# Performance work log

Hardware: AMD Instinct MI355X
Metric: run time of the kernel (lower is better)

The kernel has to match this reference:

```python
import jax, jax.numpy as jnp
import numpy as np

B, T, N = 256, 512, 256
START, STOP = 254, 255


def setup_inputs() -> dict:
    key = jax.random.key(0)
    k1, k2, k3 = jax.random.split(key, 3)
    inputs = jax.random.normal(k1, (B, T, N), dtype=jnp.float32)
    transitions = jax.random.normal(k2, (N, N), dtype=jnp.float32)
    # sentinel rows/cols as in __init__
    transitions = transitions.at[START, :].set(-10000.0).at[:, STOP].set(-10000.0)
    tags = jax.random.randint(k3, (B, T), 0, N, dtype=jnp.int32)
    mask = jnp.ones((B, T), dtype=jnp.int32)
    return {"inputs": inputs, "transitions": transitions, "tags": tags, "mask": mask}


def _input_likelihood(inputs, transitions, fmask):
    # alpha[b, tag]: log-sum over paths ending at tag
    alpha0 = transitions[:, START][None, :] + inputs[:, 0, :]

    def step(alpha, xs):
        emit, m = xs  # emit: (B, N), m: (B,)
        # inner[b, next, prev] = alpha[b, prev] + (emit[b, next] + trans[next, prev]) * mask[b, i-1]
        inner = alpha[:, None, :] + (emit[:, :, None] + transitions[None, :, :]) * m[:, None, None]
        return jax.nn.logsumexp(inner, axis=-1), None

    xs = (jnp.swapaxes(inputs[:, 1:, :], 0, 1), jnp.swapaxes(fmask[:, :-1], 0, 1))
    alpha, _ = jax.lax.scan(step, alpha0, xs)
    stops = alpha + transitions[STOP][None, :]
    return jax.nn.logsumexp(stops, axis=-1)  # (B,)


def _joint_likelihood(inputs, transitions, tags, fmask):
    score = transitions[tags[:, 0], START]  # (B,)
    # transitions[next, prev] * mask[:, i+1], summed over steps
    trans_sc = transitions[tags[:, 1:], tags[:, :-1]] * fmask[:, 1:]
    # inputs[b, i, prev_tag] * mask[:, i]
    emit_sc = jnp.take_along_axis(inputs[:, :-1, :], tags[:, :-1, None], axis=2)[..., 0] * fmask[:, :-1]
    score = score + trans_sc.sum(axis=-1) + emit_sc.sum(axis=-1)
    last_idx = (fmask.sum(axis=-1) - 1.0).astype(jnp.int32)  # (B,)
    last_tags = jnp.take_along_axis(tags, last_idx[:, None], axis=1)[:, 0]
    last_input = jnp.take_along_axis(inputs[:, -1, :], last_tags[:, None], axis=1)[:, 0]
    return score + transitions[STOP, last_tags] + last_input * fmask[:, -1]


def reference(inputs, transitions, tags, mask):
    fmask = mask.astype(jnp.float32)
    log_denominator = _input_likelihood(inputs, transitions, fmask)
    log_numerator = _joint_likelihood(inputs, transitions, tags, fmask)
    return jnp.sum(log_numerator - log_denominator)
```

## Files before the change

### kernel.cpp

```cpp
#include <hip/hip_runtime.h>
#include <hip/hip_bf16.h>
#include <stdint.h>

#define B_    256
#define T_    512
#define N_    256
#define START_ 254
#define STOP_  255
#define GCOLS 16
#define NF    16
#define ND    32
#define LOG2E 1.4426950408889634f
#define LN2   0.6931471805599453f
#define VP8   272

#define WSB_OFF 65536
#define WCF_OFF 131072
#define WCB_OFF 131328

typedef __attribute__((ext_vector_type(4))) float floatx4;

__device__ __forceinline__ void lds_barrier() {
    asm volatile("s_waitcnt lgkmcnt(0)\n\ts_barrier" ::: "memory");
}

__device__ __forceinline__ int pk_fp8x4(float a, float b, float c, float d) {
    int r = __builtin_amdgcn_cvt_pk_fp8_f32(a, b, 0, false);
    return __builtin_amdgcn_cvt_pk_fp8_f32(c, d, r, true);
}
__device__ __forceinline__ int pk_bf8x4(float a, float b, float c, float d) {
    int r = __builtin_amdgcn_cvt_pk_bf8_f32(a, b, 0, false);
    return __builtin_amdgcn_cvt_pk_bf8_f32(c, d, r, true);
}
__device__ __forceinline__ long long mk64(int lo, int hi) {
    return ((long long)(unsigned long long)(unsigned)hi << 32) | (unsigned)lo;
}

struct DenomShared {
    alignas(16) char V[2][GCOLS * VP8];
    alignas(16) float mbuf[GCOLS * 8];
    alignas(16) float sbuf[GCOLS * 8];
};

template<bool ISF>
__device__ __forceinline__ void denom_path(
    DenomShared& sh, const float* __restrict__ inputs,
    const float* __restrict__ trans, const int* __restrict__ mask,
    float* __restrict__ ws, int blkLocal)
{
    const int tid = threadIdx.x;
    const int w = tid >> 6;
    const int l = tid & 63;
    const int q = l >> 4;
    const int b = l & 15;
    const int bg = blkLocal * GCOLS + b;
    const int j0 = 32 * w + 4 * q;
    const int S = ISF ? 256 : 255;

    auto EIDX = [](int s) { return ISF ? s : (511 - s); };
    auto MIDX = [](int s) { return ISF ? (s - 1) : (511 - s); };

    long long afrag[2][8];
    #pragma unroll
    for (int mt = 0; mt < 2; ++mt) {
        const int row = 32 * w + 16 * mt + b;
        #pragma unroll
        for (int kt = 0; kt < 8; ++kt) {
            float e[8];
            if (ISF) {
                const float* p = trans + row * N_ + kt * 32 + q * 8;
                floatx4 t0 = *(const floatx4*)p;
                floatx4 t1 = *(const floatx4*)(p + 4);
                #pragma unroll
                for (int jj = 0; jj < 4; ++jj) {
                    e[jj]     = __builtin_amdgcn_exp2f(t0[jj] * LOG2E);
                    e[jj + 4] = __builtin_amdgcn_exp2f(t1[jj] * LOG2E);
                }
            } else {
                #pragma unroll
                for (int jj = 0; jj < 8; ++jj) {
                    const int k = kt * 32 + q * 8 + jj;
                    e[jj] = __builtin_amdgcn_exp2f(trans[k * N_ + row] * LOG2E);
                }
            }
            afrag[mt][kt] = mk64(pk_fp8x4(e[0], e[1], e[2], e[3]),
                                 pk_fp8x4(e[4], e[5], e[6], e[7]));
        }
    }

    const float* emitp = inputs + (size_t)bg * T_ * N_;
    const int*   maskp = mask + bg * T_;
    float C = 0.f;
    float u[2][4];

    auto produce = [&]() {
        float mx = u[0][0], sm = 0.f;
        #pragma unroll
        for (int mt = 0; mt < 2; ++mt)
            #pragma unroll
            for (int r = 0; r < 4; ++r) { mx = fmaxf(mx, u[mt][r]); sm += u[mt][r]; }
        mx = fmaxf(mx, __shfl_xor(mx, 16, 64)); sm += __shfl_xor(sm, 16, 64);
        mx = fmaxf(mx, __shfl_xor(mx, 32, 64)); sm += __shfl_xor(sm, 32, 64);
        if (l < 16) { sh.mbuf[b * 8 + w] = mx; sh.sbuf[b * 8 + w] = sm; }
    };

    if (ISF) {
        #pragma unroll
        for (int mt = 0; mt < 2; ++mt) {
            floatx4 em = *(const floatx4*)(emitp + j0 + 16 * mt);
            #pragma unroll
            for (int r = 0; r < 4; ++r) {
                const int j = j0 + 16 * mt + r;
                u[mt][r] = __builtin_amdgcn_exp2f((trans[j * N_ + START_] + em[r]) * LOG2E);
            }
        }
    } else {
        #pragma unroll
        for (int mt = 0; mt < 2; ++mt) {
            floatx4 st = *(const floatx4*)(trans + STOP_ * N_ + j0 + 16 * mt);
            #pragma unroll
            for (int r = 0; r < 4; ++r)
                u[mt][r] = __builtin_amdgcn_exp2f(st[r] * LOG2E);
        }
    }
    {
        float xpi[2][4] = {{1.f,1.f,1.f,1.f},{1.f,1.f,1.f,1.f}};
        if (!ISF) {
            #pragma unroll
            for (int mt = 0; mt < 2; ++mt) {
                floatx4 e = *(const floatx4*)(emitp + (size_t)511 * N_ + j0 + 16 * mt);
                #pragma unroll
                for (int r = 0; r < 4; ++r)
                    xpi[mt][r] = __builtin_amdgcn_exp2f(e[r] * LOG2E);
            }
        }
        produce();
        #pragma unroll
        for (int mt = 0; mt < 2; ++mt)
            *(int*)&sh.V[0][b * VP8 + j0 + 16 * mt] =
                pk_bf8x4(u[mt][0] * xpi[mt][0], u[mt][1] * xpi[mt][1],
                         u[mt][2] * xpi[mt][2], u[mt][3] * xpi[mt][3]);
    }
    floatx4 eA[2], eB[2];
    eA[0] = *(const floatx4*)(emitp + (size_t)EIDX(1) * N_ + j0);
    eA[1] = *(const floatx4*)(emitp + (size_t)EIDX(1) * N_ + j0 + 16);
    eB[0] = *(const floatx4*)(emitp + (size_t)EIDX(2) * N_ + j0);
    eB[1] = *(const floatx4*)(emitp + (size_t)EIDX(2) * N_ + j0 + 16);
    float mA = (float)maskp[MIDX(1)];
    float mB = (float)maskp[MIDX(2)];
    lds_barrier();

    auto body = [&](int s, int pr) {
        const int sp = (s + 2 <= S) ? s + 2 : S;
        floatx4 eC0 = *(const floatx4*)(emitp + (size_t)EIDX(sp) * N_ + j0);
        floatx4 eC1 = *(const floatx4*)(emitp + (size_t)EIDX(sp) * N_ + j0 + 16);
        const float mC = (float)maskp[MIDX(sp)];

        const char* vb = &sh.V[pr][b * VP8];
        long long bf[8];
        #pragma unroll
        for (int kt = 0; kt < 8; ++kt)
            bf[kt] = *(const long long*)(vb + kt * 32 + q * 8);

        floatx4 m0 = *(const floatx4*)&sh.mbuf[b * 8];
        floatx4 m1 = *(const floatx4*)&sh.mbuf[b * 8 + 4];
        floatx4 s0 = *(const floatx4*)&sh.sbuf[b * 8];
        floatx4 s1 = *(const floatx4*)&sh.sbuf[b * 8 + 4];
        const float cmax = fmaxf(fmaxf(fmaxf(m0[0], m0[1]), fmaxf(m0[2], m0[3])),
                                 fmaxf(fmaxf(m1[0], m1[1]), fmaxf(m1[2], m1[3])));
        const float csum = ((s0[0] + s0[1]) + (s0[2] + s0[3])) +
                           ((s1[0] + s1[1]) + (s1[2] + s1[3]));
        const uint32_t cb = __builtin_bit_cast(uint32_t, cmax);
        const int eb = (int)((cb >> 23) & 0xFFu);
        const float rs = __builtin_bit_cast(float, (uint32_t)(249 - eb) << 23);

        float xpv[2][4];
        #pragma unroll
        for (int r = 0; r < 4; ++r) {
            xpv[0][r] = __builtin_amdgcn_exp2f(eA[0][r] * LOG2E);
            xpv[1][r] = __builtin_amdgcn_exp2f(eA[1][r] * LOG2E);
        }

        floatx4 a0 = {0.f,0.f,0.f,0.f}, a1 = {0.f,0.f,0.f,0.f};
        floatx4 a2 = {0.f,0.f,0.f,0.f}, a3 = {0.f,0.f,0.f,0.f};
        #pragma unroll
        for (int kt = 0; kt < 4; ++kt) {
            a0 = __builtin_amdgcn_mfma_f32_16x16x32_fp8_bf8(afrag[0][kt],     bf[kt],     a0, 0, 0, 0);
            a1 = __builtin_amdgcn_mfma_f32_16x16x32_fp8_bf8(afrag[0][kt + 4], bf[kt + 4], a1, 0, 0, 0);
            a2 = __builtin_amdgcn_mfma_f32_16x16x32_fp8_bf8(afrag[1][kt],     bf[kt],     a2, 0, 0, 0);
            a3 = __builtin_amdgcn_mfma_f32_16x16x32_fp8_bf8(afrag[1][kt + 4], bf[kt + 4], a3, 0, 0, 0);
        }

        const bool live = (mA != 0.f);
        #pragma unroll
        for (int r = 0; r < 4; ++r) {
            const float v0 = a0[r] + a1[r], v1 = a2[r] + a3[r];
            u[0][r] = (live ? (ISF ? v0 * xpv[0][r] : v0) : csum) * rs;
            u[1][r] = (live ? (ISF ? v1 * xpv[1][r] : v1) : csum) * rs;
        }
        C += (float)(eb - 122);

        produce();
        #pragma unroll
        for (int mt = 0; mt < 2; ++mt) {
            *(int*)&sh.V[pr ^ 1][b * VP8 + j0 + 16 * mt] = ISF
                ? pk_bf8x4(u[mt][0], u[mt][1], u[mt][2], u[mt][3])
                : pk_bf8x4(u[mt][0] * xpv[mt][0], u[mt][1] * xpv[mt][1],
                           u[mt][2] * xpv[mt][2], u[mt][3] * xpv[mt][3]);
        }
        lds_barrier();
        eA[0] = eB[0]; eA[1] = eB[1]; eB[0] = eC0; eB[1] = eC1;
        mA = mB; mB = mC;
    };

    #pragma unroll 1
    for (int g = 0; g < 127; ++g) { body(2 * g + 1, 0); body(2 * g + 2, 1); }
    if (ISF) { body(255, 0); body(256, 1); }
    else     { body(255, 0); }

    float* wsV = ws + (ISF ? 0 : WSB_OFF);
    #pragma unroll
    for (int mt = 0; mt < 2; ++mt) {
        floatx4 vv = {u[mt][0], u[mt][1], u[mt][2], u[mt][3]};
        *(floatx4*)&wsV[(size_t)bg * N_ + j0 + 16 * mt] = vv;
    }
    if (tid < 16) {
        float* wsC = ws + (ISF ? WCF_OFF : WCB_OFF);
        wsC[blkLocal * GCOLS + tid] = C;
    }
}

__global__ __launch_bounds__(512, 2) void crf_main(
    const float* __restrict__ inputs, const float* __restrict__ trans,
    const int* __restrict__ tags, const int* __restrict__ mask,
    float* __restrict__ out, float* __restrict__ ws)
{
    __shared__ DenomShared sh;

    if (blockIdx.x >= ND) {
        float* nred = sh.mbuf;
        int*   nredi = (int*)sh.sbuf;
        const int bb = blockIdx.x - ND;
        const int t  = threadIdx.x;
        const int tg = tags[bb * T_ + t];
        const float fm = (float)mask[bb * T_ + t];
        float part = 0.f;
        if (t >= 1)      part += trans[tg * N_ + tags[bb * T_ + t - 1]] * fm;
        if (t <= T_ - 2) part += inputs[((size_t)bb * T_ + t) * N_ + tg] * fm;
        int ms = mask[bb * T_ + t];
        #pragma unroll
        for (int off = 1; off < 64; off <<= 1) {
            part += __shfl_xor(part, off, 64);
            ms   += __shfl_xor(ms, off, 64);
        }
        if ((t & 63) == 0) { nred[t >> 6] = part; nredi[t >> 6] = ms; }
        __syncthreads();
        if (t == 0) {
            float tot = 0.f; int mtot = 0;
            for (int i = 0; i < 8; ++i) { tot += nred[i]; mtot += nredi[i]; }
            tot += trans[tags[bb * T_] * N_ + START_];
            const int last = mtot - 1;
            const int lt = tags[bb * T_ + last];
            tot += trans[STOP_ * N_ + lt]
                 + inputs[((size_t)bb * T_ + (T_ - 1)) * N_ + lt]
                   * (float)mask[bb * T_ + T_ - 1];
            atomicAdd(out, tot);
        }
        return;
    }

    if (blockIdx.x < NF) denom_path<true>(sh, inputs, trans, mask, ws, blockIdx.x);
    else                 denom_path<false>(sh, inputs, trans, mask, ws, blockIdx.x - NF);
}

__global__ __launch_bounds__(256) void crf_combine(
    const float* __restrict__ ws, float* __restrict__ out)
{
    __shared__ float red[4];
    const int bb = blockIdx.x;
    const int t = threadIdx.x;
    float p = ws[(size_t)bb * N_ + t] * ws[WSB_OFF + (size_t)bb * N_ + t];
    #pragma unroll
    for (int off = 1; off < 64; off <<= 1) p += __shfl_xor(p, off, 64);
    if ((t & 63) == 0) red[t >> 6] = p;
    __syncthreads();
    if (t == 0) {
        const float tot = red[0] + red[1] + red[2] + red[3];
        const float denom = (ws[WCF_OFF + bb] + ws[WCB_OFF + bb]
                             + __builtin_amdgcn_logf(tot)) * LN2;
        atomicAdd(out, -denom);
    }
}

extern "C" void kernel_launch(void* const* d_in, const int* in_sizes, int n_in,
                              void* d_out, int out_size, void* d_ws, size_t ws_size,
                              hipStream_t stream) {
    const float* inputs = (const float*)d_in[0];
    const float* trans  = (const float*)d_in[1];
    const int*   tags   = (const int*)d_in[2];
    const int*   mask   = (const int*)d_in[3];
    float* out = (float*)d_out;
    float* ws  = (float*)d_ws;
    hipMemsetAsync(out, 0, sizeof(float), stream);
    crf_main<<<dim3(ND + B_), dim3(512), 0, stream>>>(inputs, trans, tags, mask, out, ws);
    crf_combine<<<dim3(B_), dim3(256), 0, stream>>>(ws, out);
}
```

Measured before the change: 394.2 us.

## Swizzle LDS alpha layout for 128-bit reads and trim cross-lane reduction

Reorganises the shared bf8 alpha buffer so each lane reads its eight B-fragments with four 128-bit LDS loads instead of eight 64-bit loads, using a write address that matches the MFMA operand layout. The max/sum partial reduction drops one shuffle stage, so twice as many partials go to LDS and are combined on read. In the forward path the rescale exponent is folded into the emission exp2 through an fma. The emission prefetch rotation is replaced by a two-slot ring to avoid register copies. The main risk is layout or indexing mistakes, plus somewhat more LDS reads and max/add work per step.

```diff
diff --git a/kernel.cpp b/kernel.cpp
--- a/kernel.cpp
+++ b/kernel.cpp
@@ -12,13 +12,13 @@
 #define ND    32
 #define LOG2E 1.4426950408889634f
 #define LN2   0.6931471805599453f
-#define VP8   272
 
 #define WSB_OFF 65536
 #define WCF_OFF 131072
 #define WCB_OFF 131328
 
 typedef __attribute__((ext_vector_type(4))) float floatx4;
+typedef __attribute__((ext_vector_type(2))) long long llx2;
 
 __device__ __forceinline__ void lds_barrier() {
     asm volatile("s_waitcnt lgkmcnt(0)\n\ts_barrier" ::: "memory");
@@ -37,9 +37,9 @@
 }
 
 struct DenomShared {
-    alignas(16) char V[2][GCOLS * VP8];
-    alignas(16) float mbuf[GCOLS * 8];
-    alignas(16) float sbuf[GCOLS * 8];
+    alignas(16) char  V[2][4096];
+    alignas(16) float mbuf[GCOLS * 20];
+    alignas(16) float sbuf[GCOLS * 20];
 };
 
 template<bool ISF>
@@ -59,6 +59,10 @@
 
     auto EIDX = [](int s) { return ISF ? s : (511 - s); };
     auto MIDX = [](int s) { return ISF ? (s - 1) : (511 - s); };
+
+    const int wa0 = ((w >> 1) << 10) + ((q >> 1) << 8) + (b << 4)
+                  + ((w & 1) << 3) + ((q & 1) << 2);
+    const int rbase = l << 4;
 
     long long afrag[2][8];
     #pragma unroll
@@ -99,9 +103,12 @@
         for (int mt = 0; mt < 2; ++mt)
             #pragma unroll
             for (int r = 0; r < 4; ++r) { mx = fmaxf(mx, u[mt][r]); sm += u[mt][r]; }
-        mx = fmaxf(mx, __shfl_xor(mx, 16, 64)); sm += __shfl_xor(sm, 16, 64);
-        mx = fmaxf(mx, __shfl_xor(mx, 32, 64)); sm += __shfl_xor(sm, 32, 64);
-        if (l < 16) { sh.mbuf[b * 8 + w] = mx; sh.sbuf[b * 8 + w] = sm; }
+        mx = fmaxf(mx, __shfl_xor(mx, 32, 64));
+        sm += __shfl_xor(sm, 32, 64);
+        if (l < 32) {
+            const int idx = b * 20 + w * 2 + q;
+            sh.mbuf[idx] = mx; sh.sbuf[idx] = sm;
+        }
     };
 
     if (ISF) {
@@ -137,48 +144,65 @@
         produce();
         #pragma unroll
         for (int mt = 0; mt < 2; ++mt)
-            *(int*)&sh.V[0][b * VP8 + j0 + 16 * mt] =
+            *(int*)(sh.V[0] + wa0 + (mt << 9)) =
                 pk_bf8x4(u[mt][0] * xpi[mt][0], u[mt][1] * xpi[mt][1],
                          u[mt][2] * xpi[mt][2], u[mt][3] * xpi[mt][3]);
     }
-    floatx4 eA[2], eB[2];
-    eA[0] = *(const floatx4*)(emitp + (size_t)EIDX(1) * N_ + j0);
-    eA[1] = *(const floatx4*)(emitp + (size_t)EIDX(1) * N_ + j0 + 16);
-    eB[0] = *(const floatx4*)(emitp + (size_t)EIDX(2) * N_ + j0);
-    eB[1] = *(const floatx4*)(emitp + (size_t)EIDX(2) * N_ + j0 + 16);
-    float mA = (float)maskp[MIDX(1)];
-    float mB = (float)maskp[MIDX(2)];
+    floatx4 ebuf[2][2];
+    float   mrot[2];
+    ebuf[0][0] = *(const floatx4*)(emitp + (size_t)EIDX(1) * N_ + j0);
+    ebuf[0][1] = *(const floatx4*)(emitp + (size_t)EIDX(1) * N_ + j0 + 16);
+    ebuf[1][0] = *(const floatx4*)(emitp + (size_t)EIDX(2) * N_ + j0);
+    ebuf[1][1] = *(const floatx4*)(emitp + (size_t)EIDX(2) * N_ + j0 + 16);
+    mrot[0] = (float)maskp[MIDX(1)];
+    mrot[1] = (float)maskp[MIDX(2)];
     lds_barrier();
 
-    auto body = [&](int s, int pr) {
+    auto body = [&](int s, int pr, int cur) {
         const int sp = (s + 2 <= S) ? s + 2 : S;
         floatx4 eC0 = *(const floatx4*)(emitp + (size_t)EIDX(sp) * N_ + j0);
         floatx4 eC1 = *(const floatx4*)(emitp + (size_t)EIDX(sp) * N_ + j0 + 16);
         const float mC = (float)maskp[MIDX(sp)];
 
-        const char* vb = &sh.V[pr][b * VP8];
+        const char* vb = sh.V[pr];
         long long bf[8];
         #pragma unroll
-        for (int kt = 0; kt < 8; ++kt)
-            bf[kt] = *(const long long*)(vb + kt * 32 + q * 8);
-
-        floatx4 m0 = *(const floatx4*)&sh.mbuf[b * 8];
-        floatx4 m1 = *(const floatx4*)&sh.mbuf[b * 8 + 4];
-        floatx4 s0 = *(const floatx4*)&sh.sbuf[b * 8];
-        floatx4 s1 = *(const floatx4*)&sh.sbuf[b * 8 + 4];
-        const float cmax = fmaxf(fmaxf(fmaxf(m0[0], m0[1]), fmaxf(m0[2], m0[3])),
-                                 fmaxf(fmaxf(m1[0], m1[1]), fmaxf(m1[2], m1[3])));
-        const float csum = ((s0[0] + s0[1]) + (s0[2] + s0[3])) +
-                           ((s1[0] + s1[1]) + (s1[2] + s1[3]));
+        for (int p = 0; p < 4; ++p) {
+            llx2 rd = *(const llx2*)(vb + (p << 10) + rbase);
+            bf[2 * p]     = rd[0];
+            bf[2 * p + 1] = rd[1];
+        }
+
+        const float* mb = &sh.mbuf[b * 20];
+        const float* sb = &sh.sbuf[b * 20];
+        floatx4 m0 = *(const floatx4*)mb,       m1 = *(const floatx4*)(mb + 4);
+        floatx4 m2 = *(const floatx4*)(mb + 8), m3 = *(const floatx4*)(mb + 12);
+        floatx4 s0 = *(const floatx4*)sb,       s1 = *(const floatx4*)(sb + 4);
+        floatx4 s2 = *(const floatx4*)(sb + 8), s3 = *(const floatx4*)(sb + 12);
+        float cmax = fmaxf(
+            fmaxf(fmaxf(fmaxf(m0[0], m0[1]), fmaxf(m0[2], m0[3])),
+                  fmaxf(fmaxf(m1[0], m1[1]), fmaxf(m1[2], m1[3]))),
+            fmaxf(fmaxf(fmaxf(m2[0], m2[1]), fmaxf(m2[2], m2[3])),
+                  fmaxf(fmaxf(m3[0], m3[1]), fmaxf(m3[2], m3[3]))));
+        float csum = (((s0[0] + s0[1]) + (s0[2] + s0[3])) +
+                      ((s1[0] + s1[1]) + (s1[2] + s1[3]))) +
+                     (((s2[0] + s2[1]) + (s2[2] + s2[3])) +
+                      ((s3[0] + s3[1]) + (s3[2] + s3[3])));
         const uint32_t cb = __builtin_bit_cast(uint32_t, cmax);
         const int eb = (int)((cb >> 23) & 0xFFu);
         const float rs = __builtin_bit_cast(float, (uint32_t)(249 - eb) << 23);
+        const float dCf = (float)(122 - eb);
 
         float xpv[2][4];
         #pragma unroll
         for (int r = 0; r < 4; ++r) {
-            xpv[0][r] = __builtin_amdgcn_exp2f(eA[0][r] * LOG2E);
-            xpv[1][r] = __builtin_amdgcn_exp2f(eA[1][r] * LOG2E);
+            if (ISF) {
+                xpv[0][r] = __builtin_amdgcn_exp2f(fmaf(ebuf[cur][0][r], LOG2E, dCf));
+                xpv[1][r] = __builtin_amdgcn_exp2f(fmaf(ebuf[cur][1][r], LOG2E, dCf));
+            } else {
+                xpv[0][r] = __builtin_amdgcn_exp2f(ebuf[cur][0][r] * LOG2E);
+                xpv[1][r] = __builtin_amdgcn_exp2f(ebuf[cur][1][r] * LOG2E);
+            }
         }
 
         floatx4 a0 = {0.f,0.f,0.f,0.f}, a1 = {0.f,0.f,0.f,0.f};
@@ -191,32 +215,40 @@
             a3 = __builtin_amdgcn_mfma_f32_16x16x32_fp8_bf8(afrag[1][kt + 4], bf[kt + 4], a3, 0, 0, 0);
         }
 
-        const bool live = (mA != 0.f);
+        const bool live = (mrot[cur] != 0.f);
         #pragma unroll
         for (int r = 0; r < 4; ++r) {
             const float v0 = a0[r] + a1[r], v1 = a2[r] + a3[r];
-            u[0][r] = (live ? (ISF ? v0 * xpv[0][r] : v0) : csum) * rs;
-            u[1][r] = (live ? (ISF ? v1 * xpv[1][r] : v1) : csum) * rs;
+            if (ISF) {
+                u[0][r] = live ? v0 * xpv[0][r] : csum * rs;
+                u[1][r] = live ? v1 * xpv[1][r] : csum * rs;
+            } else {
+                u[0][r] = (live ? v0 : csum) * rs;
+                u[1][r] = (live ? v1 : csum) * rs;
+            }
         }
         C += (float)(eb - 122);
 
         produce();
         #pragma unroll
         for (int mt = 0; mt < 2; ++mt) {
-            *(int*)&sh.V[pr ^ 1][b * VP8 + j0 + 16 * mt] = ISF
+            *(int*)(sh.V[pr ^ 1] + wa0 + (mt << 9)) = ISF
                 ? pk_bf8x4(u[mt][0], u[mt][1], u[mt][2], u[mt][3])
                 : pk_bf8x4(u[mt][0] * xpv[mt][0], u[mt][1] * xpv[mt][1],
                            u[mt][2] * xpv[mt][2], u[mt][3] * xpv[mt][3]);
         }
         lds_barrier();
-        eA[0] = eB[0]; eA[1] = eB[1]; eB[0] = eC0; eB[1] = eC1;
-        mA = mB; mB = mC;
+        ebuf[cur][0] = eC0; ebuf[cur][1] = eC1;
+        mrot[cur] = mC;
     };
 
     #pragma unroll 1
-    for (int g = 0; g < 127; ++g) { body(2 * g + 1, 0); body(2 * g + 2, 1); }
-    if (ISF) { body(255, 0); body(256, 1); }
-    else     { body(255, 0); }
+    for (int g = 0; g < 127; ++g) {
+        body(2 * g + 1, 0, 0);
+        body(2 * g + 2, 1, 1);
+    }
+    if (ISF) { body(255, 0, 0); body(256, 1, 1); }
+    else     { body(255, 0, 0); }
 
     float* wsV = ws + (ISF ? 0 : WSB_OFF);
     #pragma unroll
```

After: 374.8 us. -4.9%, faster.
